# Kernel tuning notes

Measured on AMD Instinct MI355X. Metric: run time of the kernel, lower is better.

Reference implementation:

```python
import jax, jax.numpy as jnp
import numpy as np

NB_CLASSES = 2048
SZ_EMBED = 128
N = 16384
TAU = 32.0
ALPHA = 0.9


def setup_inputs() -> dict:
    key = jax.random.key(0)
    k1, k2, k3 = jax.random.split(key, 3)
    X = jax.random.normal(k1, (N, SZ_EMBED), dtype=jnp.float32)
    # labels: arange % C guarantees every class occurs in the batch, so the
    # torch code's dynamic class_within_batch selection == all classes.
    T = jnp.arange(N, dtype=jnp.int64) % NB_CLASSES
    # kaiming_normal_(mode='fan_out') on [C,F]: std = sqrt(2/C)
    std = float(np.sqrt(2.0 / NB_CLASSES))
    means = jax.random.normal(k2, (NB_CLASSES, SZ_EMBED), dtype=jnp.float32) * std
    log_vars = jax.random.normal(k3, (NB_CLASSES, SZ_EMBED), dtype=jnp.float32) * std
    return {"X": X, "T": T, "means": means, "log_vars": log_vars}


def _l2norm(x, eps=1e-12):
    return x / jnp.maximum(jnp.linalg.norm(x, axis=-1, keepdims=True), eps)


def reference(X, T, means, log_vars):
    # relu6 on log-variances (torch F.relu6)
    lv = jnp.clip(log_vars, 0.0, 6.0)                      # [C,F]
    Xn = _l2norm(X)                                        # [N,F]
    mu = _l2norm(means)                                    # [C,F]
    # Mahalanobis D[n,c] = sum_f (x-mu)^2 / exp(lv)
    # Expanded to GEMMs to avoid materializing [N,C,F]:
    inv_cov = jnp.exp(-lv)                                 # [C,F]
    D = (jnp.einsum('nf,cf->nc', Xn * Xn, inv_cov)
         - 2.0 * jnp.einsum('nf,cf->nc', Xn, mu * inv_cov)
         + jnp.sum(mu * mu * inv_cov, axis=-1)[None, :])   # [N,C]
    # softmax over classes; loss_n = -log p[n, T[n]] (softmax is strictly >0,
    # so the torch `non_zero` filter keeps every row)
    logp = jax.nn.log_softmax(-TAU * D, axis=1)            # [N,C]
    loss = -logp[jnp.arange(X.shape[0]), T]                # [N]
    loss_mean = jnp.mean(loss)
    # H over all classes (all classes present in batch)
    P = jax.nn.one_hot(T, NB_CLASSES, dtype=D.dtype)       # [N,C]
    H = P + jnp.exp(-ALPHA * D) * (1.0 - P)                # [N,C]
    return (loss_mean, H)
```

## Files before the change

kernel.cpp:

```cpp
#include <hip/hip_runtime.h>

#define C_CLASSES 2048
#define F_EMBED   128
#define N_ROWS    16384

constexpr float TAU    = 32.0f;
constexpr float LOG2E  = 1.4426950408889634f;
constexpr float LN2    = 0.6931471805599453f;
constexpr float TAU2   = TAU * LOG2E;
constexpr float ZS2    = 64.0f * LOG2E;
constexpr float AL2    = -0.9f * LOG2E;

typedef __bf16 bf16x8 __attribute__((ext_vector_type(8)));
typedef float  f32x4  __attribute__((ext_vector_type(4)));

__device__ __forceinline__ float wsum64(float v) {
#pragma unroll
  for (int m = 1; m < 64; m <<= 1) v += __shfl_xor(v, m, 64);
  return v;
}

__global__ __launch_bounds__(256) void prep_classes_k(
    const float* __restrict__ means, const float* __restrict__ log_vars,
    __bf16* __restrict__ icb, __bf16* __restrict__ w2b,
    float* __restrict__ s3, float* __restrict__ out0) {
  const int c    = blockIdx.x * 4 + (threadIdx.x >> 6);
  const int lane = threadIdx.x & 63;
  const size_t base = (size_t)c * F_EMBED;
  const float m0 = means[base + lane], m1 = means[base + lane + 64];
  const float ss = wsum64(m0 * m0 + m1 * m1);
  const float inv = 1.0f / fmaxf(sqrtf(ss), 1e-12f);
  const float mu0 = m0 * inv, mu1 = m1 * inv;
  const float lv0 = fminf(fmaxf(log_vars[base + lane], 0.0f), 6.0f);
  const float lv1 = fminf(fmaxf(log_vars[base + lane + 64], 0.0f), 6.0f);
  const float ic0 = __expf(-lv0), ic1 = __expf(-lv1);
  const float s3p = wsum64(mu0 * mu0 * ic0 + mu1 * mu1 * ic1);
  icb[base + lane]      = (__bf16)ic0;
  icb[base + lane + 64] = (__bf16)ic1;
  w2b[base + lane]      = (__bf16)(-2.0f * mu0 * ic0);
  w2b[base + lane + 64] = (__bf16)(-2.0f * mu1 * ic1);
  if (lane == 0) s3[c] = s3p;
  if (c == 0 && lane == 0) out0[0] = 0.0f;
}

__global__ __launch_bounds__(256) void prep_rows_k(
    const float* __restrict__ X, __bf16* __restrict__ xnb, __bf16* __restrict__ xn2b) {
  const int n    = blockIdx.x * 4 + (threadIdx.x >> 6);
  const int lane = threadIdx.x & 63;
  const size_t base = (size_t)n * F_EMBED;
  const float x0 = X[base + lane], x1 = X[base + lane + 64];
  const float ss = wsum64(x0 * x0 + x1 * x1);
  const float inv = 1.0f / fmaxf(sqrtf(ss), 1e-12f);
  const float a0 = x0 * inv, a1 = x1 * inv;
  xnb[base + lane]       = (__bf16)a0;
  xnb[base + lane + 64]  = (__bf16)a1;
  xn2b[base + lane]      = (__bf16)(a0 * a0);
  xn2b[base + lane + 64] = (__bf16)(a1 * a1);
}

__global__ __launch_bounds__(512, 4) void mahal_main_k(
    const __bf16* __restrict__ xnb, const __bf16* __restrict__ xn2b,
    const __bf16* __restrict__ icb, const __bf16* __restrict__ w2b,
    const float* __restrict__ s3, const int* __restrict__ T,
    float* __restrict__ out) {
  __shared__ int   Tl[32];
  __shared__ float Ls[8][16];
  __shared__ float Dt[8][16];
  const int tid  = threadIdx.x;
  const int w    = tid >> 6;
  const int lane = tid & 63;
  const int lo   = lane & 15;
  const int hi   = lane >> 4;
  const int rowg = w & 1;
  const int q    = w >> 1;
  const int rowbase = blockIdx.x * 32;
  if (tid < 32) Tl[tid] = T[rowbase + tid];
  __syncthreads();

  const int myrow = rowg * 16 + lo;
  const int tTl   = Tl[myrow];

  bf16x8 axn[4], ax2[4];
  {
    const size_t rb = (size_t)(rowbase + myrow) * F_EMBED + hi * 8;
#pragma unroll
    for (int kg = 0; kg < 4; ++kg) {
      axn[kg] = *(const bf16x8*)(xnb  + rb + kg * 32);
      ax2[kg] = *(const bf16x8*)(xn2b + rb + kg * 32);
    }
  }

  float lsum = 0.0f, dTv = 0.0f;
  float* __restrict__ outH = out + 1 + (size_t)(rowbase + myrow) * C_CLASSES;

  bf16x8 cic[4], cw2[4];
  {
    const size_t cb = (size_t)(q * 64 + lo) * F_EMBED + hi * 8;
#pragma unroll
    for (int kg = 0; kg < 4; ++kg) {
      cic[kg] = *(const bf16x8*)(icb + cb + kg * 32);
      cw2[kg] = *(const bf16x8*)(w2b + cb + kg * 32);
    }
  }

  for (int t = 0; t < 32; ++t) {
    const int ctbase = (q + 4 * (t >> 2)) * 64 + (t & 3) * 16;

    f32x4 acc = {0.f, 0.f, 0.f, 0.f};
#pragma unroll
    for (int kg = 0; kg < 4; ++kg) {
      acc = __builtin_amdgcn_mfma_f32_16x16x32_bf16(cic[kg], ax2[kg], acc, 0, 0, 0);
      acc = __builtin_amdgcn_mfma_f32_16x16x32_bf16(cw2[kg], axn[kg], acc, 0, 0, 0);
    }

    if (t < 31) {
      const int t2 = t + 1;
      const int nb = (q + 4 * (t2 >> 2)) * 64 + (t2 & 3) * 16;
      const size_t cb = (size_t)(nb + lo) * F_EMBED + hi * 8;
#pragma unroll
      for (int kg = 0; kg < 4; ++kg) {
        cic[kg] = *(const bf16x8*)(icb + cb + kg * 32);
        cw2[kg] = *(const bf16x8*)(w2b + cb + kg * 32);
      }
    }

    const f32x4 s3v = *(const f32x4*)(s3 + ctbase + hi * 4);
#pragma unroll
    for (int r = 0; r < 4; ++r) {
      const int   c   = ctbase + hi * 4 + r;
      const float D   = acc[r] + s3v[r];
      const bool  isT = (c == tTl);
      outH[c] = isT ? 1.0f : exp2f(AL2 * D);
      lsum += exp2f(ZS2 - TAU2 * D);
      if (isT) dTv = D;
    }
  }

  lsum += __shfl_xor(lsum, 16, 64);
  lsum += __shfl_xor(lsum, 32, 64);
  dTv  += __shfl_xor(dTv, 16, 64);
  dTv  += __shfl_xor(dTv, 32, 64);
  if (hi == 0) { Ls[w][lo] = lsum; Dt[w][lo] = dTv; }
  __syncthreads();

  if (w == 0) {
    float loss = 0.0f;
    if (lane < 32) {
      const int rr = lane & 15, rgg = lane >> 4;
      float L = 0.f, Dv = 0.f;
#pragma unroll
      for (int qq = 0; qq < 4; ++qq) {
        L  += Ls[2 * qq + rgg][rr];
        Dv += Dt[2 * qq + rgg][rr];
      }
      loss = TAU * Dv + __log2f(L) * LN2 - 64.0f;
    }
    loss = wsum64(loss);
    if (lane == 0) atomicAdd(out, loss * (1.0f / N_ROWS));
  }
}

extern "C" void kernel_launch(void* const* d_in, const int* in_sizes, int n_in,
                              void* d_out, int out_size, void* d_ws, size_t ws_size,
                              hipStream_t stream) {
  const float* X        = (const float*)d_in[0];
  const int*   T        = (const int*)d_in[1];
  const float* means    = (const float*)d_in[2];
  const float* log_vars = (const float*)d_in[3];
  float* out = (float*)d_out;

  char* ws = (char*)d_ws;
  __bf16* icb  = (__bf16*)ws;
  __bf16* w2b  = (__bf16*)(ws + (512u << 10));
  float*  s3   = (float*)(ws + (1u << 20));
  __bf16* xnb  = (__bf16*)(ws + (1u << 20) + (16u << 10));
  __bf16* xn2b = (__bf16*)(ws + (1u << 20) + (16u << 10) + (4u << 20));

  prep_classes_k<<<C_CLASSES / 4, 256, 0, stream>>>(means, log_vars, icb, w2b, s3, out);
  prep_rows_k<<<N_ROWS / 4, 256, 0, stream>>>(X, xnb, xn2b);
  mahal_main_k<<<N_ROWS / 32, 512, 0, stream>>>(xnb, xn2b, icb, w2b, s3, T, out);
}
```

Before: 271.2 us.

## Give each wave contiguous class chunks and vectorize H stores to 16 bytes

Each wave now processes 8 contiguous 64-class chunks instead of interleaved 16-class tiles. Four 16x16 MFMA tiles are computed per chunk before the epilogue runs. The H outputs are written as 4-float vector stores instead of scalar stores, which should improve write coalescing on the dominant output traffic. The explicit next-tile prefetch is removed, so load latency is hidden only by the batched loads inside a chunk and by occupancy, and register pressure rises from the four accumulators.

After: 266.7 us. Within noise of the previous version (-1.7%).

```diff
diff --git a/kernel.cpp b/kernel.cpp
--- a/kernel.cpp
+++ b/kernel.cpp
@@ -93,46 +93,42 @@
   float lsum = 0.0f, dTv = 0.0f;
   float* __restrict__ outH = out + 1 + (size_t)(rowbase + myrow) * C_CLASSES;
 
-  bf16x8 cic[4], cw2[4];
-  {
-    const size_t cb = (size_t)(q * 64 + lo) * F_EMBED + hi * 8;
+  for (int g = 0; g < 8; ++g) {
+    const int chunk = q * 8 + g;
+    f32x4 accs[4];
+
 #pragma unroll
-    for (int kg = 0; kg < 4; ++kg) {
-      cic[kg] = *(const bf16x8*)(icb + cb + kg * 32);
-      cw2[kg] = *(const bf16x8*)(w2b + cb + kg * 32);
-    }
-  }
-
-  for (int t = 0; t < 32; ++t) {
-    const int ctbase = (q + 4 * (t >> 2)) * 64 + (t & 3) * 16;
-
-    f32x4 acc = {0.f, 0.f, 0.f, 0.f};
-#pragma unroll
-    for (int kg = 0; kg < 4; ++kg) {
-      acc = __builtin_amdgcn_mfma_f32_16x16x32_bf16(cic[kg], ax2[kg], acc, 0, 0, 0);
-      acc = __builtin_amdgcn_mfma_f32_16x16x32_bf16(cw2[kg], axn[kg], acc, 0, 0, 0);
-    }
-
-    if (t < 31) {
-      const int t2 = t + 1;
-      const int nb = (q + 4 * (t2 >> 2)) * 64 + (t2 & 3) * 16;
-      const size_t cb = (size_t)(nb + lo) * F_EMBED + hi * 8;
+    for (int s = 0; s < 4; ++s) {
+      const size_t cb = (size_t)(chunk * 64 + s * 16 + lo) * F_EMBED + hi * 8;
+      bf16x8 cic[4], cw2[4];
 #pragma unroll
       for (int kg = 0; kg < 4; ++kg) {
         cic[kg] = *(const bf16x8*)(icb + cb + kg * 32);
         cw2[kg] = *(const bf16x8*)(w2b + cb + kg * 32);
       }
+      f32x4 acc = {0.f, 0.f, 0.f, 0.f};
+#pragma unroll
+      for (int kg = 0; kg < 4; ++kg) {
+        acc = __builtin_amdgcn_mfma_f32_16x16x32_bf16(cic[kg], ax2[kg], acc, 0, 0, 0);
+        acc = __builtin_amdgcn_mfma_f32_16x16x32_bf16(cw2[kg], axn[kg], acc, 0, 0, 0);
+      }
+      accs[s] = acc;
     }
 
-    const f32x4 s3v = *(const f32x4*)(s3 + ctbase + hi * 4);
 #pragma unroll
-    for (int r = 0; r < 4; ++r) {
-      const int   c   = ctbase + hi * 4 + r;
-      const float D   = acc[r] + s3v[r];
-      const bool  isT = (c == tTl);
-      outH[c] = isT ? 1.0f : exp2f(AL2 * D);
-      lsum += exp2f(ZS2 - TAU2 * D);
-      if (isT) dTv = D;
+    for (int s = 0; s < 4; ++s) {
+      const int cb0 = chunk * 64 + s * 16 + hi * 4;
+      const f32x4 s3v = *(const f32x4*)(s3 + cb0);
+      f32x4 hv;
+#pragma unroll
+      for (int r = 0; r < 4; ++r) {
+        const float D   = accs[s][r] + s3v[r];
+        const bool  isT = (cb0 + r == tTl);
+        hv[r] = isT ? 1.0f : exp2f(AL2 * D);
+        lsum += exp2f(ZS2 - TAU2 * D);
+        if (isT) dTv = D;
+      }
+      __builtin_memcpy(outH + cb0, &hv, 16);
     }
   }
 
```
